# Optimization experiments

Measured on AMD Instinct MI355X. Metric: run time of the kernel, lower is better.

## Reference

```python
import jax, jax.numpy as jnp
import numpy as np

B, HW, D, CL, K, V, NL, H = 16, 4096, 512, 768, 512, 512, 32, 8
EPS = 1e-5

def conv1d(x, w, b):
    # 1x1 Conv1d: x (B, Cin, L), w (Cout, Cin), b (Cout,)
    return jnp.einsum('oi,bil->bol', w, x) + b[:, None]

def inorm(x):
    # InstanceNorm1d (affine=False, biased var) over the length dim per channel
    m = jnp.mean(x, axis=-1, keepdims=True)
    v = jnp.var(x, axis=-1, keepdims=True)
    return (x - m) / jnp.sqrt(v + EPS)

def _forward(x, l, l_mask, w_vis, b_vis, w_langp, b_langp, w_q, b_q, w_k, b_k,
             w_v, b_v, w_lv, b_lv, w_W, b_W, w_langW, b_langW,
             w_mm, b_mm, w_langmm, b_langmm):
    xt = x.transpose(0, 2, 1)                       # (B, D, HW)
    mask = l_mask.transpose(0, 2, 1)                # (B, 1, NL)
    vis = jax.nn.gelu(conv1d(xt, w_vis, b_vis), approximate=False)      # (B, D, HW)
    lang = jax.nn.gelu(conv1d(l, w_langp, b_langp), approximate=False)  # (B, CL, NL)

    q = inorm(conv1d(xt, w_q, b_q)).transpose(0, 2, 1)   # (B, HW, K)
    k = conv1d(l, w_k, b_k) * mask                       # (B, K, NL)
    v = conv1d(l, w_v, b_v) * mask                       # (B, V, NL)
    lv = inorm(conv1d(xt, w_lv, b_lv))                   # (B, CL, HW)

    q = q.reshape(B, HW, H, K // H).transpose(0, 2, 1, 3)   # (B, H, HW, dk)
    k = k.reshape(B, H, K // H, NL)
    v = v.reshape(B, H, V // H, NL)
    lv = lv.reshape(B, H, CL // H, HW)

    # note: scale uses FULL key_channels (as in the torch code), mask bias added once
    sim = jnp.einsum('bhqd,bhdn->bhqn', q, k) * (K ** -0.5)
    sim = sim + (10000.0 * mask[:, :, None, :] - 10000.0)    # (B, H, HW, NL)

    att = jax.nn.softmax(sim, axis=-1)                         # image -> lang
    latt = jax.nn.softmax(sim.transpose(0, 1, 3, 2), axis=-1)  # lang -> image

    lang_out = jnp.einsum('bhnq,bhcq->bhcn', latt, lv).reshape(B, CL, NL) * mask
    lang_out = inorm(conv1d(lang_out, w_langW, b_langW))       # (B, CL, NL)

    out = jnp.einsum('bhqn,bhdn->bqhd', att, v).reshape(B, HW, V)
    vis_out = inorm(conv1d(out.transpose(0, 2, 1), w_W, b_W))  # (B, V, HW)

    mm = jax.nn.gelu(conv1d(vis * vis_out, w_mm, b_mm), approximate=False)
    lang_mm = jax.nn.gelu(conv1d(lang * lang_out, w_langmm, b_langmm), approximate=False)
    return mm.transpose(0, 2, 1), lang_mm.transpose(0, 2, 1)   # (B,HW,V), (B,NL,CL)

def setup_inputs():
    key = jax.random.key(0)
    ks = jax.random.split(key, 24)
    inp = {}
    inp['x'] = jax.random.normal(ks[0], (B, HW, D), jnp.float32)
    inp['l'] = jax.random.normal(ks[1], (B, CL, NL), jnp.float32)
    lengths = jax.random.randint(ks[2], (B, 1), 5, NL + 1)
    inp['l_mask'] = (jnp.arange(NL)[None, :] < lengths).astype(jnp.float32)[:, :, None]
    specs = [('vis', D, D), ('langp', CL, CL), ('q', K, D), ('k', K, CL),
             ('v', V, CL), ('lv', CL, D), ('W', V, V), ('langW', CL, CL),
             ('mm', V, V), ('langmm', CL, CL)]
    for i, (n, o, ci) in enumerate(specs):
        inp['w_' + n] = jax.random.normal(ks[3 + 2 * i], (o, ci), jnp.float32) / float(np.sqrt(ci))
        inp['b_' + n] = jax.random.normal(ks[4 + 2 * i], (o,), jnp.float32) * 0.01
    return inp

def reference(x, l, l_mask, w_vis, b_vis, w_langp, b_langp, w_q, b_q, w_k, b_k,
              w_v, b_v, w_lv, b_lv, w_W, b_W, w_langW, b_langW,
              w_mm, b_mm, w_langmm, b_langmm):
    return _forward(x, l, l_mask, w_vis, b_vis, w_langp, b_langp, w_q, b_q, w_k, b_k,
                    w_v, b_v, w_lv, b_lv, w_W, b_W, w_langW, b_langW,
                    w_mm, b_mm, w_langmm, b_langmm)
```

## Files before the change

kernel.cpp:

```cpp
#include <hip/hip_runtime.h>
#include <cstdint>
#include <cstddef>


typedef __bf16 bf16x8 __attribute__((ext_vector_type(8)));
typedef float f32x4 __attribute__((ext_vector_type(4)));
typedef unsigned short ushort8 __attribute__((ext_vector_type(8)));
typedef unsigned short us4 __attribute__((ext_vector_type(4)));

__device__ __forceinline__ float bf2f(unsigned short u) {
  union { unsigned int i; float f; } c; c.i = ((unsigned int)u) << 16; return c.f;
}
__device__ __forceinline__ unsigned short f2bf(float f) {
  union { float f; unsigned int i; } c; c.f = f;
  unsigned int r = c.i + 0x7FFFu + ((c.i >> 16) & 1u);
  return (unsigned short)(r >> 16);
}
__device__ __forceinline__ float gelu_f(float x) {
  return 0.5f * x * (1.f + erff(x * 0.70710678118654752f));
}
__device__ __forceinline__ void gload16(const void* g, void* l) {
  __builtin_amdgcn_global_load_lds(
      (__attribute__((address_space(1))) unsigned int*)g,
      (__attribute__((address_space(3))) unsigned int*)l, 16, 0, 0);
}
__device__ __forceinline__ int xcd_swizzle(int orig, int nwg) {
  int qd = nwg >> 3, r = nwg & 7;
  int xcd = orig & 7, idx = orig >> 3;
  return (xcd < r ? xcd * (qd + 1) : r * (qd + 1) + (xcd - r) * qd) + idx;
}

constexpr size_t OFF_SRQ  = 0;
constexpr size_t OFF_SRLV = OFF_SRQ  + (size_t)16*512*2*4;
constexpr size_t OFF_SRW  = OFF_SRLV + (size_t)16*768*2*4;
constexpr size_t OFF_LACC = OFF_SRW  + (size_t)16*512*2*4;
constexpr size_t SZ_ZERO  = OFF_LACC + (size_t)16*768*32*4;
constexpr size_t OFF_KBUF = SZ_ZERO;
constexpr size_t OFF_VBUF = OFF_KBUF + (size_t)16*512*32*4;
constexpr size_t OFF_LANG = OFF_VBUF + (size_t)16*512*32*4;
constexpr size_t OFF_P2   = OFF_LANG + (size_t)16*768*32*4;
constexpr size_t OFF_PMX  = OFF_P2   + (size_t)16*768*32*4;
constexpr size_t OFF_PSM  = OFF_PMX  + (size_t)32*128*32*4;
constexpr size_t OFF_WB   = OFF_PSM  + (size_t)32*128*32*4;
constexpr size_t OFF_Q    = OFF_WB   + (size_t)1441792*2;
constexpr size_t OFF_LV   = OFF_Q    + (size_t)65536*512*2;
constexpr size_t OFF_SIMB = OFF_LV   + (size_t)65536*768*2;

__global__ __launch_bounds__(256) void prep_kernel(
    const float* __restrict__ x,
    const float* __restrict__ w_vis, const float* __restrict__ w_q,
    const float* __restrict__ w_lv, const float* __restrict__ w_W,
    const float* __restrict__ w_mm,
    unsigned short* __restrict__ xb, unsigned short* __restrict__ wb,
    const float* __restrict__ l,
    const float* __restrict__ w_langp, const float* __restrict__ b_langp,
    const float* __restrict__ w_k, const float* __restrict__ b_k,
    const float* __restrict__ w_v, const float* __restrict__ b_v,
    const float* __restrict__ lmask,
    float* __restrict__ lang, float* __restrict__ kbuf, float* __restrict__ vbuf,
    float* __restrict__ zbase)
{
  const int bid = blockIdx.x, t = threadIdx.x;
  if (bid < 17088) {
    int i = bid * 256 + t;
    if (i >= 4374528) return;
    const float* src;
    unsigned short* dst;
    if (i < 4194304) { src = x + (size_t)i * 8; dst = xb + (size_t)i * 8; }
    else {
      int j = i - 4194304;
      dst = wb + (size_t)j * 8;
      if (j < 32768)       src = w_vis + (size_t)j * 8;
      else if (j < 65536)  src = w_q  + (size_t)(j - 32768) * 8;
      else if (j < 114688) src = w_lv + (size_t)(j - 65536) * 8;
      else if (j < 147456) src = w_W  + (size_t)(j - 114688) * 8;
      else                 src = w_mm + (size_t)(j - 147456) * 8;
    }
    const f32x4* s = (const f32x4*)src;
    f32x4 a = s[0], b2 = s[1];
    ushort8 o;
#pragma unroll
    for (int j = 0; j < 4; ++j) { o[j] = f2bf(a[j]); o[j + 4] = f2bf(b2[j]); }
    *(ushort8*)dst = o;
  } else if (bid < 20672) {
    int sb = bid - 17088;
    int b = sb & 15, og = sb >> 4;
    int ol = t >> 5, n = t & 31;
    const float* lb = l + (size_t)b * 768 * 32 + n;
    const float* wr;
    float bv;
    float* out;
    bool gel;
    if (og < 96) {
      int o = og * 8 + ol;
      wr = w_langp + (size_t)o * 768; bv = b_langp[o];
      out = &lang[((size_t)b * 768 + o) * 32 + n]; gel = true;
    } else if (og < 160) {
      int o = (og - 96) * 8 + ol;
      wr = w_k + (size_t)o * 768; bv = b_k[o];
      out = &kbuf[((size_t)b * 512 + o) * 32 + n]; gel = false;
    } else {
      int o = (og - 160) * 8 + ol;
      wr = w_v + (size_t)o * 768; bv = b_v[o];
      out = &vbuf[((size_t)b * 512 + o) * 32 + n]; gel = false;
    }
    float s = 0.f;
#pragma unroll 4
    for (int i = 0; i < 768; ++i) s += wr[i] * lb[(size_t)i * 32];
    s += bv;
    s = gel ? gelu_f(s) : s * lmask[b * 32 + n];
    *out = s;
  } else {
    size_t i = (size_t)(bid - 20672) * 256 + t;
    const f32x4 z = {0.f, 0.f, 0.f, 0.f};
    ((f32x4*)zbase)[i] = z;
  }
}

template<bool GELU, bool STATS, bool OUTF32>
__global__ __launch_bounds__(256) void gemm_bt(
    const unsigned short* __restrict__ A, const unsigned short* __restrict__ Wb,
    const float* __restrict__ bias, void* __restrict__ Yout,
    float* __restrict__ statsraw, int N, int Kd, int nbn)
{
  __shared__ __align__(16) unsigned short As[128 * 64];
  __shared__ __align__(16) unsigned short Bs[128 * 64];
  const int t = threadIdx.x;
  const int wave = t >> 6, lane = t & 63;
  const int ln = lane & 15, quad = lane >> 4;
  const int wgid = xcd_swizzle(blockIdx.x, gridDim.x);
  const int mt = wgid / nbn, nt = wgid - mt * nbn;
  const int m0 = mt * 128, n0 = nt * 128;
  const int wm = (wave >> 1) * 64, wn = (wave & 1) * 64;
  const f32x4 fzero = {0.f, 0.f, 0.f, 0.f};
  f32x4 acc[4][4];
#pragma unroll
  for (int i = 0; i < 4; ++i)
#pragma unroll
    for (int j = 0; j < 4; ++j) acc[i][j] = fzero;
  const int lrow = lane >> 3;
  const int lch  = lane & 7;

  for (int k0 = 0; k0 < Kd; k0 += 64) {
#pragma unroll
    for (int it = 0; it < 4; ++it) {
      int g = wave * 4 + it;
      int row = g * 8 + lrow;
      gload16(A  + (size_t)(m0 + row) * Kd + k0 + lch * 8, &As[g * 512]);
      gload16(Wb + (size_t)(n0 + row) * Kd + k0 + lch * 8, &Bs[g * 512]);
    }
    __syncthreads();
#pragma unroll
    for (int kk = 0; kk < 64; kk += 32) {
      int c = (kk >> 3) + quad;
      bf16x8 af[4], bfr[4];
#pragma unroll
      for (int i = 0; i < 4; ++i)
        af[i] = *(const bf16x8*)&As[(wm + i * 16 + ln) * 64 + c * 8];
#pragma unroll
      for (int j = 0; j < 4; ++j)
        bfr[j] = *(const bf16x8*)&Bs[(wn + j * 16 + ln) * 64 + c * 8];
#pragma unroll
      for (int i = 0; i < 4; ++i)
#pragma unroll
        for (int j = 0; j < 4; ++j)
          acc[i][j] = __builtin_amdgcn_mfma_f32_16x16x32_bf16(af[i], bfr[j], acc[i][j], 0, 0, 0);
    }
    __syncthreads();
  }
  float bb[4];
#pragma unroll
  for (int j = 0; j < 4; ++j) bb[j] = bias[n0 + wn + j * 16 + ln];
#pragma unroll
  for (int i = 0; i < 4; ++i)
#pragma unroll
    for (int j = 0; j < 4; ++j)
#pragma unroll
      for (int r = 0; r < 4; ++r) {
        float v = acc[i][j][r] + bb[j];
        if (GELU) v = gelu_f(v);
        acc[i][j][r] = v;
        size_t row = (size_t)(m0 + wm + i * 16 + quad * 4 + r);
        size_t idx = row * N + (n0 + wn + j * 16 + ln);
        if (OUTF32) ((float*)Yout)[idx] = v;
        else ((unsigned short*)Yout)[idx] = f2bf(v);
      }
  if (STATS) {
    float* cs = (float*)As;
    cs[t] = 0.f;
    __syncthreads();
#pragma unroll
    for (int j = 0; j < 4; ++j) {
      float s = 0.f, s2 = 0.f;
#pragma unroll
      for (int i = 0; i < 4; ++i)
#pragma unroll
        for (int r = 0; r < 4; ++r) { float v = acc[i][j][r]; s += v; s2 += v * v; }
      s  += __shfl_xor(s, 16);  s  += __shfl_xor(s, 32);
      s2 += __shfl_xor(s2, 16); s2 += __shfl_xor(s2, 32);
      if (quad == 0) {
        int cl = wn + j * 16 + ln;
        atomicAdd(&cs[cl], s);
        atomicAdd(&cs[128 + cl], s2);
      }
    }
    __syncthreads();
    int bIdx = m0 >> 12;
    if (t < 128) atomicAdd(&statsraw[((size_t)bIdx * N + n0 + t) * 2], cs[t]);
    else atomicAdd(&statsraw[((size_t)bIdx * N + n0 + (t - 128)) * 2 + 1], cs[t]);
  }
}

__global__ __launch_bounds__(256) void gemm_fused3(
    const unsigned short* __restrict__ A, const unsigned short* __restrict__ Wcat,
    const float* __restrict__ b_vis, const float* __restrict__ b_q, const float* __restrict__ b_lv,
    unsigned short* __restrict__ visb, unsigned short* __restrict__ qout,
    unsigned short* __restrict__ lvout, float* __restrict__ srq, float* __restrict__ srlv)
{
  constexpr int NBN = 14, Kd = 512;
  __shared__ __align__(16) unsigned short As[128 * 64];
  __shared__ __align__(16) unsigned short Bs[128 * 64];
  const int t = threadIdx.x;
  const int wave = t >> 6, lane = t & 63;
  const int ln = lane & 15, quad = lane >> 4;
  const int wgid = xcd_swizzle(blockIdx.x, gridDim.x);
  const int mt = wgid / NBN, nt = wgid - mt * NBN;
  const int m0 = mt * 128, n0 = nt * 128;
  const int wm = (wave >> 1) * 64, wn = (wave & 1) * 64;
  const f32x4 fzero = {0.f, 0.f, 0.f, 0.f};
  f32x4 acc[4][4];
#pragma unroll
  for (int i = 0; i < 4; ++i)
#pragma unroll
    for (int j = 0; j < 4; ++j) acc[i][j] = fzero;
  const int lrow = lane >> 3;
  const int lch  = lane & 7;

  for (int k0 = 0; k0 < Kd; k0 += 64) {
#pragma unroll
    for (int it = 0; it < 4; ++it) {
      int g = wave * 4 + it;
      int row = g * 8 + lrow;
      gload16(A    + (size_t)(m0 + row) * Kd + k0 + lch * 8, &As[g * 512]);
      gload16(Wcat + (size_t)(n0 + row) * Kd + k0 + lch * 8, &Bs[g * 512]);
    }
    __syncthreads();
#pragma unroll
    for (int kk = 0; kk < 64; kk += 32) {
      int c = (kk >> 3) + quad;
      bf16x8 af[4], bfr[4];
#pragma unroll
      for (int i = 0; i < 4; ++i)
        af[i] = *(const bf16x8*)&As[(wm + i * 16 + ln) * 64 + c * 8];
#pragma unroll
      for (int j = 0; j < 4; ++j)
        bfr[j] = *(const bf16x8*)&Bs[(wn + j * 16 + ln) * 64 + c * 8];
#pragma unroll
      for (int i = 0; i < 4; ++i)
#pragma unroll
        for (int j = 0; j < 4; ++j)
          acc[i][j] = __builtin_amdgcn_mfma_f32_16x16x32_bf16(af[i], bfr[j], acc[i][j], 0, 0, 0);
    }
    __syncthreads();
  }
  int seg = (nt < 4) ? 0 : (nt < 8 ? 1 : 2);
  const float* bias = (seg == 0) ? b_vis : (seg == 1 ? b_q : b_lv);
  unsigned short* Y = (seg == 0) ? visb : (seg == 1 ? qout : lvout);
  float* statsraw   = (seg == 1) ? srq : srlv;
  const int nbase   = n0 - ((seg == 0) ? 0 : (seg == 1 ? 512 : 1024));
  const int Nseg    = (seg == 2) ? 768 : 512;

  float bb[4];
#pragma unroll
  for (int j = 0; j < 4; ++j) bb[j] = bias[nbase + wn + j * 16 + ln];
#pragma unroll
  for (int i = 0; i < 4; ++i)
#pragma unroll
    for (int j = 0; j < 4; ++j)
#pragma unroll
      for (int r = 0; r < 4; ++r) {
        float v = acc[i][j][r] + bb[j];
        if (seg == 0) v = gelu_f(v);
        acc[i][j][r] = v;
        size_t row = (size_t)(m0 + wm + i * 16 + quad * 4 + r);
        Y[row * Nseg + (nbase + wn + j * 16 + ln)] = f2bf(v);
      }
  if (seg != 0) {
    float* cs = (float*)As;
    cs[t] = 0.f;
    __syncthreads();
#pragma unroll
    for (int j = 0; j < 4; ++j) {
      float s = 0.f, s2 = 0.f;
#pragma unroll
      for (int i = 0; i < 4; ++i)
#pragma unroll
        for (int r = 0; r < 4; ++r) { float v = acc[i][j][r]; s += v; s2 += v * v; }
      s  += __shfl_xor(s, 16);  s  += __shfl_xor(s, 32);
      s2 += __shfl_xor(s2, 16); s2 += __shfl_xor(s2, 32);
      if (quad == 0) {
        int cl = wn + j * 16 + ln;
        atomicAdd(&cs[cl], s);
        atomicAdd(&cs[128 + cl], s2);
      }
    }
    __syncthreads();
    int bIdx = m0 >> 12;
    if (t < 128) atomicAdd(&statsraw[((size_t)bIdx * Nseg + nbase + t) * 2], cs[t]);
    else atomicAdd(&statsraw[((size_t)bIdx * Nseg + nbase + (t - 128)) * 2 + 1], cs[t]);
  }
}

__global__ __launch_bounds__(256) void simattv_kernel(
    const unsigned short* __restrict__ qraw, const float* __restrict__ srq,
    const float* __restrict__ kbuf, const float* __restrict__ vbuf,
    const float* __restrict__ lmask,
    unsigned short* __restrict__ simb, unsigned short* __restrict__ outb,
    float* __restrict__ pmx, float* __restrict__ psm)
{
  __shared__ __align__(16) unsigned short kThi[32][72];
  __shared__ __align__(16) unsigned short kTlo[32][72];
  __shared__ __align__(16) unsigned short vshi[64][40];
  __shared__ __align__(16) unsigned short vslo[64][40];
  __shared__ __align__(16) unsigned short pq[4][32][40];
  __shared__ float sm[64], srs[64], cb[32];
  __shared__ float wmax[4][32], wsum[4][32];

  const int qc = blockIdx.x, q0 = qc * 128, h = blockIdx.y, b = blockIdx.z;
  const int bh = b * 8 + h;
  const int t = threadIdx.x;
  const int wv = t >> 6, lane = t & 63, ln = lane & 15, quad = lane >> 4;
  const float scale = 0.04419417382415922f;

  if (t < 64) {
    float s  = srq[(b * 512 + h * 64 + t) * 2];
    float s2 = srq[(b * 512 + h * 64 + t) * 2 + 1];
    float mean = s * (1.f / 4096.f);
    float var  = fmaxf(s2 * (1.f / 4096.f) - mean * mean, 0.f);
    sm[t]  = mean;
    srs[t] = rsqrtf(var + 1e-5f) * scale;
  }
  __syncthreads();

  const float* kb = kbuf + ((size_t)b * 512 + h * 64) * 32;
  const float* vb = vbuf + ((size_t)b * 512 + h * 64) * 32;
  for (int e = t; e < 2048; e += 256) {
    int d = e >> 5, n = e & 31;
    float kv = kb[e] * srs[d];
    unsigned short khi = f2bf(kv);
    kThi[n][d] = khi;
    kTlo[n][d] = f2bf(kv - bf2f(khi));
    float vv = vb[e];
    unsigned short vhi = f2bf(vv);
    vshi[d][n] = vhi;
    vslo[d][n] = f2bf(vv - bf2f(vhi));
  }
  if (t < 32) {
    float s = 0.f;
#pragma unroll 8
    for (int d = 0; d < 64; ++d) s += sm[d] * srs[d] * kb[d * 32 + t];
    cb[t] = 10000.f * (lmask[b * 32 + t] - 1.f) - s;
  }

  const unsigned short* qbase = qraw + ((size_t)(b * 4096) + q0 + wv * 32) * 512 + h * 64;
  bf16x8 qfr[2][2];
#pragma unroll
  for (int qf = 0; qf < 2; ++qf)
#pragma unroll
    for (int kf = 0; kf < 2; ++kf)
      qfr[qf][kf] = *(const bf16x8*)(qbase + (size_t)(qf * 16 + ln) * 512 + kf * 32 + quad * 8);
  __syncthreads();

  const f32x4 fz = {0.f, 0.f, 0.f, 0.f};
  f32x4 accS[2][2] = {{fz, fz}, {fz, fz}};
#pragma unroll
  for (int kf = 0; kf < 2; ++kf) {
#pragma unroll
    for (int nf = 0; nf < 2; ++nf) {
      bf16x8 kh = *(const bf16x8*)&kThi[nf * 16 + ln][kf * 32 + quad * 8];
      bf16x8 kl = *(const bf16x8*)&kTlo[nf * 16 + ln][kf * 32 + quad * 8];
#pragma unroll
      for (int qf = 0; qf < 2; ++qf) {
        accS[qf][nf] = __builtin_amdgcn_mfma_f32_16x16x32_bf16(qfr[qf][kf], kh, accS[qf][nf], 0, 0, 0);
        accS[qf][nf] = __builtin_amdgcn_mfma_f32_16x16x32_bf16(qfr[qf][kf], kl, accS[qf][nf], 0, 0, 0);
      }
    }
  }
  float cb0 = cb[ln], cb1 = cb[16 + ln];
#pragma unroll
  for (int qf = 0; qf < 2; ++qf)
#pragma unroll
    for (int r = 0; r < 4; ++r) {
      accS[qf][0][r] += cb0;
      accS[qf][1][r] += cb1;
    }
  {
    unsigned short* sgb = simb + ((size_t)bh * 4096 + q0 + wv * 32) * 32;
#pragma unroll
    for (int qf = 0; qf < 2; ++qf)
#pragma unroll
      for (int r = 0; r < 4; ++r) {
        size_t rowo = (size_t)(qf * 16 + quad * 4 + r) * 32;
        sgb[rowo + ln]      = f2bf(accS[qf][0][r]);
        sgb[rowo + 16 + ln] = f2bf(accS[qf][1][r]);
      }
  }
#pragma unroll
  for (int nf = 0; nf < 2; ++nf) {
    float m = accS[0][nf][0];
#pragma unroll
    for (int r = 1; r < 4; ++r) m = fmaxf(m, accS[0][nf][r]);
#pragma unroll
    for (int r = 0; r < 4; ++r) m = fmaxf(m, accS[1][nf][r]);
    m = fmaxf(m, __shfl_xor(m, 16));
    m = fmaxf(m, __shfl_xor(m, 32));
    float s = 0.f;
#pragma unroll
    for (int qf = 0; qf < 2; ++qf)
#pragma unroll
      for (int r = 0; r < 4; ++r) s += __expf(accS[qf][nf][r] - m);
    s += __shfl_xor(s, 16);
    s += __shfl_xor(s, 32);
    if (quad == 0) { wmax[wv][nf * 16 + ln] = m; wsum[wv][nf * 16 + ln] = s; }
  }
#pragma unroll
  for (int qf = 0; qf < 2; ++qf) {
#pragma unroll
    for (int r = 0; r < 4; ++r) {
      float a0 = accS[qf][0][r], a1 = accS[qf][1][r];
      float m = fmaxf(a0, a1);
      m = fmaxf(m, __shfl_xor(m, 1));
      m = fmaxf(m, __shfl_xor(m, 2));
      m = fmaxf(m, __shfl_xor(m, 4));
      m = fmaxf(m, __shfl_xor(m, 8));
      float e0 = __expf(a0 - m), e1 = __expf(a1 - m);
      float s = e0 + e1;
      s += __shfl_xor(s, 1);
      s += __shfl_xor(s, 2);
      s += __shfl_xor(s, 4);
      s += __shfl_xor(s, 8);
      float inv = 1.f / s;
      int row = qf * 16 + quad * 4 + r;
      pq[wv][row][ln]      = f2bf(e0 * inv);
      pq[wv][row][16 + ln] = f2bf(e1 * inv);
    }
  }
  __syncthreads();
  bf16x8 vfh[4], vfl[4];
#pragma unroll
  for (int mf = 0; mf < 4; ++mf) {
    vfh[mf] = *(const bf16x8*)&vshi[mf * 16 + ln][quad * 8];
    vfl[mf] = *(const bf16x8*)&vslo[mf * 16 + ln][quad * 8];
  }
#pragma unroll
  for (int nf = 0; nf < 2; ++nf) {
    bf16x8 pb = *(const bf16x8*)&pq[wv][nf * 16 + ln][quad * 8];
    f32x4 accO[4] = {fz, fz, fz, fz};
#pragma unroll
    for (int mf = 0; mf < 4; ++mf) {
      accO[mf] = __builtin_amdgcn_mfma_f32_16x16x32_bf16(vfh[mf], pb, accO[mf], 0, 0, 0);
      accO[mf] = __builtin_amdgcn_mfma_f32_16x16x32_bf16(vfl[mf], pb, accO[mf], 0, 0, 0);
    }
    unsigned short* op = outb + ((size_t)(b * 4096) + q0 + wv * 32 + nf * 16 + ln) * 512 + h * 64;
#pragma unroll
    for (int mf = 0; mf < 4; ++mf) {
      us4 o;
#pragma unroll
      for (int r = 0; r < 4; ++r) o[r] = f2bf(accO[mf][r]);
      *(us4*)(op + mf * 16 + quad * 4) = o;
    }
  }
  __syncthreads();
  if (t < 32) {
    float M = wmax[0][t], S = wsum[0][t];
#pragma unroll
    for (int g = 1; g < 4; ++g) {
      float m2 = wmax[g][t], s2 = wsum[g][t];
      if (m2 > M) { S = S * __expf(M - m2) + s2; M = m2; }
      else S += s2 * __expf(m2 - M);
    }
    pmx[((size_t)qc * 128 + bh) * 32 + t] = M;
    psm[((size_t)qc * 128 + bh) * 32 + t] = S;
  }
}

__global__ __launch_bounds__(256) void langout_acc_kernel(
    const unsigned short* __restrict__ simb, const float* __restrict__ pmx,
    const float* __restrict__ psm, const unsigned short* __restrict__ lvraw,
    const float* __restrict__ srlv, float* __restrict__ lacc)
{
  __shared__ __align__(16) float pt[64][32];
  __shared__ __align__(16) float lvt[64][96];
  __shared__ float cm[96], cr[96], lm[32], li[32];
  int bh = blockIdx.x, b = bh >> 3, h = bh & 7;
  int qs0 = blockIdx.y * 512;
  int t = threadIdx.x;
  if (t < 96) {
    float s  = srlv[(b * 768 + h * 96 + t) * 2];
    float s2 = srlv[(b * 768 + h * 96 + t) * 2 + 1];
    float mean = s * (1.f / 4096.f);
    float var  = fmaxf(s2 * (1.f / 4096.f) - mean * mean, 0.f);
    cm[t] = mean;
    cr[t] = rsqrtf(var + 1e-5f);
  } else if (t >= 128 && t < 160) {
    int n = t - 128;
    float M = -1e30f, S = 0.f;
#pragma unroll 4
    for (int c = 0; c < 32; ++c) {
      float m2 = pmx[((size_t)c * 128 + bh) * 32 + n];
      float s2 = psm[((size_t)c * 128 + bh) * 32 + n];
      if (m2 > M) { S = S * __expf(M - m2) + s2; M = m2; }
      else S += s2 * __expf(m2 - M);
    }
    lm[n] = M;
    li[n] = 1.f / S;
  }
  __syncthreads();
  int n = t & 31, cg = t >> 5;
  float acc[12];
#pragma unroll
  for (int r = 0; r < 12; ++r) acc[r] = 0.f;
  for (int c0 = 0; c0 < 512; c0 += 64) {
    if (c0) __syncthreads();
#pragma unroll
    for (int i = 0; i < 8; ++i) {
      int e = t + 256 * i;
      int ql = e >> 5, nn = e & 31;
      float x = bf2f(simb[((size_t)bh * 4096 + qs0 + c0 + ql) * 32 + nn]);
      pt[ql][nn] = __expf(x - lm[nn]) * li[nn];
    }
#pragma unroll
    for (int i = 0; i < 24; ++i) {
      int e = t + 256 * i;
      int ql = e / 96, cc = e % 96;
      float v = bf2f(lvraw[((size_t)(b * 4096) + qs0 + c0 + ql) * 768 + h * 96 + cc]);
      lvt[ql][cc] = (v - cm[cc]) * cr[cc];
    }
    __syncthreads();
    for (int q = 0; q < 64; ++q) {
      float pv = pt[q][n];
      const f32x4* lp = (const f32x4*)&lvt[q][cg * 12];
      f32x4 a0 = lp[0], a1 = lp[1], a2 = lp[2];
      acc[0] += pv * a0[0]; acc[1] += pv * a0[1]; acc[2]  += pv * a0[2]; acc[3]  += pv * a0[3];
      acc[4] += pv * a1[0]; acc[5] += pv * a1[1]; acc[6]  += pv * a1[2]; acc[7]  += pv * a1[3];
      acc[8] += pv * a2[0]; acc[9] += pv * a2[1]; acc[10] += pv * a2[2]; acc[11] += pv * a2[3];
    }
  }
#pragma unroll
  for (int r = 0; r < 12; ++r)
    atomicAdd(&lacc[((size_t)b * 768 + h * 96 + cg * 12 + r) * 32 + n], acc[r]);
}

__global__ __launch_bounds__(256) void prod_kernel(
    const unsigned short* __restrict__ visb, const unsigned short* __restrict__ wraw,
    const float* __restrict__ srw, unsigned short* __restrict__ P)
{
  size_t idx = ((size_t)blockIdx.x * 256 + threadIdx.x) * 8;
  int b = (int)(idx >> 21);
  int c = (int)(idx & 511);
  ushort8 vv = *(const ushort8*)&visb[idx];
  ushort8 wv = *(const ushort8*)&wraw[idx];
  ushort8 pv;
#pragma unroll
  for (int i = 0; i < 8; ++i) {
    float s  = srw[(b * 512 + c + i) * 2];
    float s2 = srw[(b * 512 + c + i) * 2 + 1];
    float mean = s * (1.f / 4096.f);
    float var  = fmaxf(s2 * (1.f / 4096.f) - mean * mean, 0.f);
    float rs   = rsqrtf(var + 1e-5f);
    pv[i] = f2bf(bf2f(vv[i]) * ((bf2f(wv[i]) - mean) * rs));
  }
  *(ushort8*)&P[idx] = pv;
}

__global__ __launch_bounds__(256) void langW_kernel(
    const float* __restrict__ lacc, const float* __restrict__ w,
    const float* __restrict__ bias, const float* __restrict__ lmask,
    const float* __restrict__ lang, float* __restrict__ p2)
{
  int b = blockIdx.x, og = blockIdx.y;
  int ol = threadIdx.x >> 5, n = threadIdx.x & 31;
  int o = og * 8 + ol;
  const float* ab = lacc + (size_t)b * 768 * 32 + n;
  const float* wr = w + (size_t)o * 768;
  float s = 0.f;
#pragma unroll 4
  for (int i = 0; i < 768; ++i) s += wr[i] * ab[(size_t)i * 32];
  float y = s * lmask[b * 32 + n] + bias[o];
  float m = y;
#pragma unroll
  for (int off = 16; off >= 1; off >>= 1) m += __shfl_xor(m, off);
  m *= (1.f / 32.f);
  float d = y - m;
  float vv = d * d;
#pragma unroll
  for (int off = 16; off >= 1; off >>= 1) vv += __shfl_xor(vv, off);
  vv *= (1.f / 32.f);
  size_t idx = ((size_t)b * 768 + o) * 32 + n;
  p2[idx] = lang[idx] * (d * rsqrtf(vv + 1e-5f));
}

__global__ __launch_bounds__(256) void langmm_kernel(
    const float* __restrict__ p2, const float* __restrict__ w,
    const float* __restrict__ bias, float* __restrict__ out1)
{
  int b = blockIdx.x, og = blockIdx.y;
  int ol = threadIdx.x >> 5, n = threadIdx.x & 31;
  int o = og * 8 + ol;
  const float* pb = p2 + (size_t)b * 768 * 32 + n;
  const float* wr = w + (size_t)o * 768;
  float s = 0.f;
#pragma unroll 4
  for (int i = 0; i < 768; ++i) s += wr[i] * pb[(size_t)i * 32];
  s = gelu_f(s + bias[o]);
  __shared__ float tile[8][32];
  tile[ol][n] = s;
  __syncthreads();
  int nn = threadIdx.x >> 3, cl = threadIdx.x & 7;
  out1[((size_t)b * 32 + nn) * 768 + og * 8 + cl] = tile[cl][nn];
}

extern "C" void kernel_launch(void* const* d_in, const int* in_sizes, int n_in,
                              void* d_out, int out_size, void* d_ws, size_t ws_size,
                              hipStream_t stream)
{
  (void)in_sizes; (void)n_in; (void)out_size; (void)ws_size;
  const float* x       = (const float*)d_in[0];
  const float* l       = (const float*)d_in[1];
  const float* lmask   = (const float*)d_in[2];
  const float* w_vis   = (const float*)d_in[3];
  const float* b_vis   = (const float*)d_in[4];
  const float* w_langp = (const float*)d_in[5];
  const float* b_langp = (const float*)d_in[6];
  const float* w_q     = (const float*)d_in[7];
  const float* b_q     = (const float*)d_in[8];
  const float* w_k     = (const float*)d_in[9];
  const float* b_k     = (const float*)d_in[10];
  const float* w_v     = (const float*)d_in[11];
  const float* b_v     = (const float*)d_in[12];
  const float* w_lv    = (const float*)d_in[13];
  const float* b_lv    = (const float*)d_in[14];
  const float* w_W     = (const float*)d_in[15];
  const float* b_W     = (const float*)d_in[16];
  const float* w_langW = (const float*)d_in[17];
  const float* b_langW = (const float*)d_in[18];
  const float* w_mm    = (const float*)d_in[19];
  const float* b_mm    = (const float*)d_in[20];
  const float* w_langmm= (const float*)d_in[21];
  const float* b_langmm= (const float*)d_in[22];

  char* ws = (char*)d_ws;
  float* srq  = (float*)(ws + OFF_SRQ);
  float* srlv = (float*)(ws + OFF_SRLV);
  float* srw  = (float*)(ws + OFF_SRW);
  float* lacc = (float*)(ws + OFF_LACC);
  float* kbuf = (float*)(ws + OFF_KBUF);
  float* vbuf = (float*)(ws + OFF_VBUF);
  float* lang = (float*)(ws + OFF_LANG);
  float* p2   = (float*)(ws + OFF_P2);
  float* pmx  = (float*)(ws + OFF_PMX);
  float* psm  = (float*)(ws + OFF_PSM);
  unsigned short* wb    = (unsigned short*)(ws + OFF_WB);
  unsigned short* wbW   = wb + 917504;
  unsigned short* wbmm  = wb + 1179648;
  unsigned short* qraw  = (unsigned short*)(ws + OFF_Q);
  unsigned short* lvraw = (unsigned short*)(ws + OFF_LV);
  unsigned short* wraw  = (unsigned short*)(ws + OFF_LV);
  unsigned short* simb  = (unsigned short*)(ws + OFF_SIMB);
  float* out0 = (float*)d_out;
  float* out1 = out0 + (size_t)16 * 4096 * 512;
  unsigned short* visb = (unsigned short*)d_out;
  unsigned short* xb   = (unsigned short*)d_out + 33554432;

  prep_kernel<<<21112, 256, 0, stream>>>(x, w_vis, w_q, w_lv, w_W, w_mm, xb, wb,
                                         l, w_langp, b_langp, w_k, b_k, w_v, b_v,
                                         lmask, lang, kbuf, vbuf, (float*)ws);

  gemm_fused3<<<512 * 14, 256, 0, stream>>>(xb, wb, b_vis, b_q, b_lv,
                                            visb, qraw, lvraw, srq, srlv);

  simattv_kernel<<<dim3(32, 8, 16), 256, 0, stream>>>(qraw, srq, kbuf, vbuf, lmask, simb, qraw, pmx, psm);
  langout_acc_kernel<<<dim3(128, 8), 256, 0, stream>>>(simb, pmx, psm, lvraw, srlv, lacc);

  gemm_bt<false, true,  false><<<512 * 4, 256, 0, stream>>>(qraw, wbW, b_W, wraw, srw, 512, 512, 4);
  prod_kernel<<<16384, 256, 0, stream>>>(visb, wraw, srw, qraw);
  gemm_bt<true,  false, true ><<<512 * 4, 256, 0, stream>>>(qraw, wbmm, b_mm, out0, nullptr, 512, 512, 4);

  langW_kernel<<<dim3(16, 96), 256, 0, stream>>>(lacc, w_langW, b_langW, lmask, lang, p2);
  langmm_kernel<<<dim3(16, 96), 256, 0, stream>>>(p2, w_langmm, b_langmm, out1);
}
```

Before: 1.319 ms.

## Double-buffer LDS tiles in bf16 GEMM kernels to overlap loads with MFMA

```diff
diff --git a/kernel.cpp b/kernel.cpp
--- a/kernel.cpp
+++ b/kernel.cpp
@@ -123,8 +123,8 @@
     const float* __restrict__ bias, void* __restrict__ Yout,
     float* __restrict__ statsraw, int N, int Kd, int nbn)
 {
-  __shared__ __align__(16) unsigned short As[128 * 64];
-  __shared__ __align__(16) unsigned short Bs[128 * 64];
+  __shared__ __align__(16) unsigned short As[2][128 * 64];
+  __shared__ __align__(16) unsigned short Bs[2][128 * 64];
   const int t = threadIdx.x;
   const int wave = t >> 6, lane = t & 63;
   const int ln = lane & 15, quad = lane >> 4;
@@ -140,26 +140,35 @@
     for (int j = 0; j < 4; ++j) acc[i][j] = fzero;
   const int lrow = lane >> 3;
   const int lch  = lane & 7;
-
-  for (int k0 = 0; k0 < Kd; k0 += 64) {
-#pragma unroll
-    for (int it = 0; it < 4; ++it) {
-      int g = wave * 4 + it;
-      int row = g * 8 + lrow;
-      gload16(A  + (size_t)(m0 + row) * Kd + k0 + lch * 8, &As[g * 512]);
-      gload16(Wb + (size_t)(n0 + row) * Kd + k0 + lch * 8, &Bs[g * 512]);
-    }
-    __syncthreads();
+  const unsigned short* Arow = A  + (size_t)(m0 + wave * 32 + lrow) * Kd + lch * 8;
+  const unsigned short* Brow = Wb + (size_t)(n0 + wave * 32 + lrow) * Kd + lch * 8;
+
+#define STAGE_BT(buf, k0)                                                     \
+  {                                                                           \
+    _Pragma("unroll")                                                         \
+    for (int it = 0; it < 4; ++it) {                                          \
+      int g = wave * 4 + it;                                                  \
+      gload16(Arow + (size_t)(it * 8) * Kd + (k0), &As[buf][g * 512]);        \
+      gload16(Brow + (size_t)(it * 8) * Kd + (k0), &Bs[buf][g * 512]);        \
+    }                                                                         \
+  }
+
+  const int NT = Kd >> 6;
+  STAGE_BT(0, 0)
+  __syncthreads();
+  int cur = 0;
+  for (int kt = 0; kt < NT; ++kt) {
+    if (kt + 1 < NT) STAGE_BT(cur ^ 1, (kt + 1) * 64)
 #pragma unroll
     for (int kk = 0; kk < 64; kk += 32) {
       int c = (kk >> 3) + quad;
       bf16x8 af[4], bfr[4];
 #pragma unroll
       for (int i = 0; i < 4; ++i)
-        af[i] = *(const bf16x8*)&As[(wm + i * 16 + ln) * 64 + c * 8];
+        af[i] = *(const bf16x8*)&As[cur][(wm + i * 16 + ln) * 64 + c * 8];
 #pragma unroll
       for (int j = 0; j < 4; ++j)
-        bfr[j] = *(const bf16x8*)&Bs[(wn + j * 16 + ln) * 64 + c * 8];
+        bfr[j] = *(const bf16x8*)&Bs[cur][(wn + j * 16 + ln) * 64 + c * 8];
 #pragma unroll
       for (int i = 0; i < 4; ++i)
 #pragma unroll
@@ -167,6 +176,7 @@
           acc[i][j] = __builtin_amdgcn_mfma_f32_16x16x32_bf16(af[i], bfr[j], acc[i][j], 0, 0, 0);
     }
     __syncthreads();
+    cur ^= 1;
   }
   float bb[4];
 #pragma unroll
@@ -218,8 +228,8 @@
     unsigned short* __restrict__ lvout, float* __restrict__ srq, float* __restrict__ srlv)
 {
   constexpr int NBN = 14, Kd = 512;
-  __shared__ __align__(16) unsigned short As[128 * 64];
-  __shared__ __align__(16) unsigned short Bs[128 * 64];
+  __shared__ __align__(16) unsigned short As[2][128 * 64];
+  __shared__ __align__(16) unsigned short Bs[2][128 * 64];
   const int t = threadIdx.x;
   const int wave = t >> 6, lane = t & 63;
   const int ln = lane & 15, quad = lane >> 4;
@@ -235,26 +245,25 @@
     for (int j = 0; j < 4; ++j) acc[i][j] = fzero;
   const int lrow = lane >> 3;
   const int lch  = lane & 7;
-
-  for (int k0 = 0; k0 < Kd; k0 += 64) {
-#pragma unroll
-    for (int it = 0; it < 4; ++it) {
-      int g = wave * 4 + it;
-      int row = g * 8 + lrow;
-      gload16(A    + (size_t)(m0 + row) * Kd + k0 + lch * 8, &As[g * 512]);
-      gload16(Wcat + (size_t)(n0 + row) * Kd + k0 + lch * 8, &Bs[g * 512]);
-    }
-    __syncthreads();
+  const unsigned short* Arow = A    + (size_t)(m0 + wave * 32 + lrow) * Kd + lch * 8;
+  const unsigned short* Brow = Wcat + (size_t)(n0 + wave * 32 + lrow) * Kd + lch * 8;
+
+  constexpr int NT = Kd >> 6;
+  STAGE_BT(0, 0)
+  __syncthreads();
+  int cur = 0;
+  for (int kt = 0; kt < NT; ++kt) {
+    if (kt + 1 < NT) STAGE_BT(cur ^ 1, (kt + 1) * 64)
 #pragma unroll
     for (int kk = 0; kk < 64; kk += 32) {
       int c = (kk >> 3) + quad;
       bf16x8 af[4], bfr[4];
 #pragma unroll
       for (int i = 0; i < 4; ++i)
-        af[i] = *(const bf16x8*)&As[(wm + i * 16 + ln) * 64 + c * 8];
+        af[i] = *(const bf16x8*)&As[cur][(wm + i * 16 + ln) * 64 + c * 8];
 #pragma unroll
       for (int j = 0; j < 4; ++j)
-        bfr[j] = *(const bf16x8*)&Bs[(wn + j * 16 + ln) * 64 + c * 8];
+        bfr[j] = *(const bf16x8*)&Bs[cur][(wn + j * 16 + ln) * 64 + c * 8];
 #pragma unroll
       for (int i = 0; i < 4; ++i)
 #pragma unroll
@@ -262,6 +271,7 @@
           acc[i][j] = __builtin_amdgcn_mfma_f32_16x16x32_bf16(af[i], bfr[j], acc[i][j], 0, 0, 0);
     }
     __syncthreads();
+    cur ^= 1;
   }
   int seg = (nt < 4) ? 0 : (nt < 8 ? 1 : 2);
   const float* bias = (seg == 0) ? b_vis : (seg == 1 ? b_q : b_lv);
```

New measurement: 1.216 ms. 7.9% less time.
